# Kernel optimization log

Hardware: AMD Instinct MI355X
Metric: run time of the kernel (lower is better)

Reference implementation:

```python
import jax, jax.numpy as jnp
import numpy as np

B, L, D = 8, 128, 768
DEP, POS = 64, 64
OUT = 768
NEG = -1e30


def setup_inputs() -> dict:
    key = jax.random.key(0)
    ks = jax.random.split(key, 12)
    fan = DEP + POS + D
    s_attn = 1.0 / np.sqrt(fan)
    inp = {
        "text": jax.random.normal(ks[0], (B, L, D), jnp.float32),
        "adj": jax.random.randint(ks[1], (B, L, L), 0, 2, jnp.int32),
        "dep_embed": jax.random.normal(ks[2], (B, L, L, DEP), jnp.float32),
        "pos_embed": jax.random.normal(ks[3], (B, L, POS), jnp.float32),
        # dep_attn Linear(dep+pos+in -> out), split into the three column blocks
        # of the concat order [text | pos | dep]
        "Wt": jax.random.normal(ks[4], (D, OUT), jnp.float32) * s_attn,
        "Wp_attn": jax.random.normal(ks[5], (POS, OUT), jnp.float32) * s_attn,
        "Wd_attn": jax.random.normal(ks[6], (DEP, OUT), jnp.float32) * s_attn,
        "b_attn": jax.random.normal(ks[7], (OUT,), jnp.float32) * s_attn,
        # dep_fc Linear(dep -> out)
        "Wd": jax.random.normal(ks[8], (DEP, OUT), jnp.float32) / np.sqrt(DEP),
        "bd": jax.random.normal(ks[9], (OUT,), jnp.float32) / np.sqrt(DEP),
        # pos_fc Linear(pos -> out)
        "Wp": jax.random.normal(ks[10], (POS, OUT), jnp.float32) / np.sqrt(POS),
        "bp": jax.random.normal(ks[11], (OUT,), jnp.float32) / np.sqrt(POS),
    }
    return inp


def reference(text, adj, dep_embed, pos_embed, Wt, Wp_attn, Wd_attn, b_attn, Wd, bd, Wp, bp):
    # dep_attn(cat([val_us, pos_us, dep_embed])) == sum of per-block linears,
    # with the text/pos parts broadcast along the j (neighbor) axis.
    r = (jnp.einsum('bid,do->bio', text, Wt)[:, :, None, :]
         + jnp.einsum('bip,po->bio', pos_embed, Wp_attn)[:, :, None, :]
         + jnp.einsum('bijd,do->bijo', dep_embed, Wd_attn)
         + b_attn)                                    # [B, L, L, OUT]
    scores = jnp.sum(r, axis=-1) + jnp.where(adj == 0, NEG, 0.0)
    p = jax.nn.softmax(scores, axis=2)                # [B, L, L]
    # output = val_us + pos_fc(pos_us) + dep_fc(dep_embed); weighted-sum over j
    msg = (text[:, :, None, :]
           + (pos_embed @ Wp + bp)[:, :, None, :]
           + jnp.einsum('bijd,do->bijo', dep_embed, Wd) + bd)  # [B, L, L, D]
    output_sum = jnp.einsum('bij,bijo->bio', p, msg)  # [B, L, D]
    return r, output_sum, p
```

## Files before the change

### kernel.cpp

```cpp
#include <hip/hip_runtime.h>
#include <hip/hip_bf16.h>

typedef float v4f __attribute__((ext_vector_type(4)));

__global__ __launch_bounds__(256) void k_wdsum(const float* __restrict__ Wda,
                                               float* __restrict__ wd_sum) {
    int k = blockIdx.x, t = threadIdx.x;
    float s = Wda[k * 768 + t] + Wda[k * 768 + 256 + t] + Wda[k * 768 + 512 + t];
#pragma unroll
    for (int off = 32; off; off >>= 1) s += __shfl_down(s, off, 64);
    __shared__ float red[4];
    if ((t & 63) == 0) red[t >> 6] = s;
    __syncthreads();
    if (t == 0) wd_sum[k] = red[0] + red[1] + red[2] + red[3];
}

__global__ __launch_bounds__(256) void k_tattn(const float* __restrict__ text,
                                               const float* __restrict__ pos,
                                               const float* __restrict__ Wt,
                                               const float* __restrict__ Wpa,
                                               const float* __restrict__ b_attn,
                                               float* __restrict__ t_attn) {
    __shared__ float At[64][68];
    __shared__ float Bt[64][64];
    int t = threadIdx.x;
    int M0 = blockIdx.x * 64, N0 = blockIdx.y * 64;
    int r0 = (t >> 4) * 4, o0 = (t & 15) * 4;
    float acc[16] = {};
    for (int kc = 0; kc < 13; ++kc) {
        __syncthreads();
        for (int f = t * 4; f < 4096; f += 1024) {
            int row = f >> 6, kcol = f & 63;
            float4 v;
            if (kc < 12) v = *(const float4*)&text[(size_t)(M0 + row) * 768 + kc * 64 + kcol];
            else         v = *(const float4*)&pos[(size_t)(M0 + row) * 64 + kcol];
            At[kcol + 0][row] = v.x; At[kcol + 1][row] = v.y;
            At[kcol + 2][row] = v.z; At[kcol + 3][row] = v.w;
        }
        for (int f = t * 4; f < 4096; f += 1024) {
            int kr = f >> 6, oc = f & 63;
            float4 v;
            if (kc < 12) v = *(const float4*)&Wt[(size_t)(kc * 64 + kr) * 768 + N0 + oc];
            else         v = *(const float4*)&Wpa[(size_t)kr * 768 + N0 + oc];
            *(float4*)&Bt[kr][oc] = v;
        }
        __syncthreads();
#pragma unroll 8
        for (int k = 0; k < 64; ++k) {
            float4 a = *(const float4*)&At[k][r0];
            float4 b = *(const float4*)&Bt[k][o0];
            float av[4] = {a.x, a.y, a.z, a.w};
            float bv[4] = {b.x, b.y, b.z, b.w};
#pragma unroll
            for (int i = 0; i < 4; ++i)
#pragma unroll
                for (int j = 0; j < 4; ++j) acc[i * 4 + j] += av[i] * bv[j];
        }
    }
    float4 bias = *(const float4*)&b_attn[N0 + o0];
    float bb[4] = {bias.x, bias.y, bias.z, bias.w};
#pragma unroll
    for (int i = 0; i < 4; ++i) {
        float4 o;
        o.x = acc[i * 4 + 0] + bb[0]; o.y = acc[i * 4 + 1] + bb[1];
        o.z = acc[i * 4 + 2] + bb[2]; o.w = acc[i * 4 + 3] + bb[3];
        *(float4*)&t_attn[(size_t)(M0 + r0 + i) * 768 + N0 + o0] = o;
    }
}

__global__ __launch_bounds__(256) void k_mega(const float* __restrict__ dep,
                                              const int* __restrict__ adj,
                                              const float* __restrict__ Wda,
                                              const float* __restrict__ t_attn,
                                              const float* __restrict__ wd_sum,
                                              float* __restrict__ r_out,
                                              float* __restrict__ out_p,
                                              float* __restrict__ pd_out) {
    __shared__ float dt[64][132];
    __shared__ float wb[64][64];
    __shared__ float wds[64];
    __shared__ float sc[128];
    __shared__ float pv[128];
    __shared__ float pdp[4][64];
    __shared__ float red[8];
    int t = threadIdx.x;
    int bi = blockIdx.x;
    const float* depb = dep + (size_t)bi * (128 * 64);
    for (int f = t * 4; f < 8192; f += 1024) {
        int j = f >> 6, k0 = f & 63;
        float4 v = *(const float4*)&depb[f];
        dt[k0 + 0][j] = v.x; dt[k0 + 1][j] = v.y;
        dt[k0 + 2][j] = v.z; dt[k0 + 3][j] = v.w;
    }
    if (t < 64) wds[t] = wd_sum[t];
    const float* ta = t_attn + (size_t)bi * 768;
    float s = ta[t] + ta[t + 256] + ta[t + 512];
#pragma unroll
    for (int off = 32; off; off >>= 1) s += __shfl_down(s, off, 64);
    if ((t & 63) == 0) red[t >> 6] = s;
    __syncthreads();
    float S_t = red[0] + red[1] + red[2] + red[3];
    if (t < 128) {
        float d = 0.f;
#pragma unroll
        for (int k = 0; k < 64; ++k) d += dt[k][t] * wds[k];
        float v = S_t + d;
        if (adj[(size_t)bi * 128 + t] == 0) v += -1e30f;
        sc[t] = v;
    }
    __syncthreads();
    if (t < 64) {
        float v = fmaxf(sc[t], sc[t + 64]);
#pragma unroll
        for (int off = 32; off; off >>= 1) v = fmaxf(v, __shfl_down(v, off, 64));
        if (t == 0) red[4] = v;
    }
    __syncthreads();
    if (t < 128) pv[t] = __expf(sc[t] - red[4]);
    __syncthreads();
    if (t < 64) {
        float v = pv[t] + pv[t + 64];
#pragma unroll
        for (int off = 32; off; off >>= 1) v += __shfl_down(v, off, 64);
        if (t == 0) red[5] = v;
    }
    __syncthreads();
    float inv = 1.0f / red[5];
    if (t < 128) {
        float pj = pv[t] * inv;
        pv[t] = pj;
        out_p[(size_t)bi * 128 + t] = pj;
    }
    __syncthreads();
    {
        int k = t & 63, seg = t >> 6;
        float a = 0.f;
#pragma unroll
        for (int jj = 0; jj < 32; ++jj) a += pv[seg * 32 + jj] * dt[k][seg * 32 + jj];
        pdp[seg][k] = a;
    }
    __syncthreads();
    if (t < 64) pd_out[(size_t)bi * 64 + t] = pdp[0][t] + pdp[1][t] + pdp[2][t] + pdp[3][t];

    int j0 = (t >> 3) * 4;
    int o0 = (t & 7) * 8;
    float* rb = r_out + (size_t)bi * (128 * 768);
    for (int oc = 0; oc < 12; ++oc) {
        __syncthreads();
        for (int f = t * 4; f < 4096; f += 1024) {
            int k = f >> 6, o = f & 63;
            *(float4*)&wb[k][o] = *(const float4*)&Wda[(size_t)k * 768 + oc * 64 + o];
        }
        __syncthreads();
        float acc[32] = {};
#pragma unroll 4
        for (int k = 0; k < 64; ++k) {
            float4 a  = *(const float4*)&dt[k][j0];
            float4 b0 = *(const float4*)&wb[k][o0];
            float4 b1 = *(const float4*)&wb[k][o0 + 4];
            float av[4] = {a.x, a.y, a.z, a.w};
            float bv[8] = {b0.x, b0.y, b0.z, b0.w, b1.x, b1.y, b1.z, b1.w};
#pragma unroll
            for (int jj = 0; jj < 4; ++jj)
#pragma unroll
                for (int oo = 0; oo < 8; ++oo) acc[jj * 8 + oo] += av[jj] * bv[oo];
        }
        float4 t0 = *(const float4*)&ta[oc * 64 + o0];
        float4 t1 = *(const float4*)&ta[oc * 64 + o0 + 4];
        float tv[8] = {t0.x, t0.y, t0.z, t0.w, t1.x, t1.y, t1.z, t1.w};
#pragma unroll
        for (int jj = 0; jj < 4; ++jj) {
            float* dst = &rb[(size_t)(j0 + jj) * 768 + oc * 64 + o0];
            v4f w0 = {acc[jj * 8 + 0] + tv[0], acc[jj * 8 + 1] + tv[1],
                      acc[jj * 8 + 2] + tv[2], acc[jj * 8 + 3] + tv[3]};
            v4f w1 = {acc[jj * 8 + 4] + tv[4], acc[jj * 8 + 5] + tv[5],
                      acc[jj * 8 + 6] + tv[6], acc[jj * 8 + 7] + tv[7]};
            __builtin_nontemporal_store(w0, (v4f*)dst);
            __builtin_nontemporal_store(w1, (v4f*)(dst + 4));
        }
    }
}

__global__ __launch_bounds__(256) void k_out(const float* __restrict__ text,
                                             const float* __restrict__ pos,
                                             const float* __restrict__ Wp,
                                             const float* __restrict__ bp,
                                             const float* __restrict__ Wd,
                                             const float* __restrict__ bd,
                                             const float* __restrict__ pd,
                                             float* __restrict__ outp) {
    __shared__ float ps[8][64];
    __shared__ float pdl[8][64];
    int t = threadIdx.x;
    int bi0 = blockIdx.x * 8;
    for (int f = t; f < 512; f += 256) {
        int g = f >> 6, k = f & 63;
        ps[g][k]  = pos[(size_t)(bi0 + g) * 64 + k];
        pdl[g][k] = pd[(size_t)(bi0 + g) * 64 + k];
    }
    __syncthreads();
    if (t < 192) {
        int d0 = t * 4;
        float acc[32] = {};
#pragma unroll 4
        for (int k = 0; k < 64; ++k) {
            float4 wp = *(const float4*)&Wp[(size_t)k * 768 + d0];
            float4 wd = *(const float4*)&Wd[(size_t)k * 768 + d0];
            float wpv[4] = {wp.x, wp.y, wp.z, wp.w};
            float wdv[4] = {wd.x, wd.y, wd.z, wd.w};
#pragma unroll
            for (int g = 0; g < 8; ++g) {
                float pk = ps[g][k], dk = pdl[g][k];
#pragma unroll
                for (int c = 0; c < 4; ++c) acc[g * 4 + c] += pk * wpv[c] + dk * wdv[c];
            }
        }
        float4 bpv = *(const float4*)&bp[d0];
        float4 bdv = *(const float4*)&bd[d0];
        float bb[4] = {bpv.x + bdv.x, bpv.y + bdv.y, bpv.z + bdv.z, bpv.w + bdv.w};
#pragma unroll
        for (int g = 0; g < 8; ++g) {
            float4 tx = *(const float4*)&text[(size_t)(bi0 + g) * 768 + d0];
            float4 o;
            o.x = acc[g * 4 + 0] + tx.x + bb[0];
            o.y = acc[g * 4 + 1] + tx.y + bb[1];
            o.z = acc[g * 4 + 2] + tx.z + bb[2];
            o.w = acc[g * 4 + 3] + tx.w + bb[3];
            *(float4*)&outp[(size_t)(bi0 + g) * 768 + d0] = o;
        }
    }
}

extern "C" void kernel_launch(void* const* d_in, const int* in_sizes, int n_in,
                              void* d_out, int out_size, void* d_ws, size_t ws_size,
                              hipStream_t stream) {
    const float* text   = (const float*)d_in[0];
    const int*   adj    = (const int*)d_in[1];
    const float* dep    = (const float*)d_in[2];
    const float* pos    = (const float*)d_in[3];
    const float* Wt     = (const float*)d_in[4];
    const float* Wpa    = (const float*)d_in[5];
    const float* Wda    = (const float*)d_in[6];
    const float* b_attn = (const float*)d_in[7];
    const float* Wd     = (const float*)d_in[8];
    const float* bd     = (const float*)d_in[9];
    const float* Wp     = (const float*)d_in[10];
    const float* bp     = (const float*)d_in[11];

    float* out    = (float*)d_out;
    float* r_out  = out;
    float* os_out = out + (size_t)8 * 128 * 128 * 768;
    float* p_out  = os_out + (size_t)8 * 128 * 768;

    float* ws     = (float*)d_ws;
    float* t_attn = ws;
    float* wd_sum = ws + 786432;
    float* pd     = ws + 786496;

    k_wdsum<<<64, 256, 0, stream>>>(Wda, wd_sum);
    k_tattn<<<dim3(16, 12), 256, 0, stream>>>(text, pos, Wt, Wpa, b_attn, t_attn);
    k_mega<<<1024, 256, 0, stream>>>(dep, adj, Wda, t_attn, wd_sum, r_out, p_out, pd);
    k_out<<<128, 256, 0, stream>>>(text, pos, Wp, bp, Wd, bd, pd, os_out);
}
```

Baseline: 651.2 us.

## Compute dependency-attention projection with bf16 MFMA instead of scalar FP32 FMA

The big dep_embed × Wd_attn product that writes r now runs on bf16 MFMA 16x16x32 instructions. A new pre-pass converts and transposes Wd_attn to bf16, and dep_embed is staged in LDS as bf16. The score and pooled-dep reductions now read fp32 dep straight from global memory, dropping the fp32 transposed LDS tile and the per-chunk weight staging and barriers. Output stores become scalar nontemporal stores in MFMA layout, and using bf16 lowers accuracy, which may exceed the tolerance for r.

After: 621.0 us. 4.6% less time.

```diff
diff --git a/kernel.cpp b/kernel.cpp
--- a/kernel.cpp
+++ b/kernel.cpp
@@ -2,6 +2,13 @@
 #include <hip/hip_bf16.h>
 
 typedef float v4f __attribute__((ext_vector_type(4)));
+typedef short short8 __attribute__((ext_vector_type(8)));
+
+__device__ inline ushort f2bf(float x) {
+    unsigned u = __float_as_uint(x);
+    unsigned r = u + 0x7fffu + ((u >> 16) & 1u);
+    return (ushort)(r >> 16);
+}
 
 __global__ __launch_bounds__(256) void k_wdsum(const float* __restrict__ Wda,
                                                float* __restrict__ wd_sum) {
@@ -13,6 +20,13 @@
     if ((t & 63) == 0) red[t >> 6] = s;
     __syncthreads();
     if (t == 0) wd_sum[k] = red[0] + red[1] + red[2] + red[3];
+}
+
+__global__ __launch_bounds__(256) void k_cvt(const float* __restrict__ Wda,
+                                             ushort* __restrict__ wdat) {
+    int idx = blockIdx.x * 256 + threadIdx.x;
+    int o = idx >> 6, k = idx & 63;
+    wdat[idx] = f2bf(Wda[(size_t)k * 768 + o]);
 }
 
 __global__ __launch_bounds__(256) void k_tattn(const float* __restrict__ text,
@@ -70,14 +84,13 @@
 
 __global__ __launch_bounds__(256) void k_mega(const float* __restrict__ dep,
                                               const int* __restrict__ adj,
-                                              const float* __restrict__ Wda,
+                                              const ushort* __restrict__ wdat,
                                               const float* __restrict__ t_attn,
                                               const float* __restrict__ wd_sum,
                                               float* __restrict__ r_out,
                                               float* __restrict__ out_p,
                                               float* __restrict__ pd_out) {
-    __shared__ float dt[64][132];
-    __shared__ float wb[64][64];
+    __shared__ __align__(16) ushort db[128 * 72];
     __shared__ float wds[64];
     __shared__ float sc[128];
     __shared__ float pv[128];
@@ -86,11 +99,15 @@
     int t = threadIdx.x;
     int bi = blockIdx.x;
     const float* depb = dep + (size_t)bi * (128 * 64);
-    for (int f = t * 4; f < 8192; f += 1024) {
-        int j = f >> 6, k0 = f & 63;
-        float4 v = *(const float4*)&depb[f];
-        dt[k0 + 0][j] = v.x; dt[k0 + 1][j] = v.y;
-        dt[k0 + 2][j] = v.z; dt[k0 + 3][j] = v.w;
+#pragma unroll
+    for (int it = 0; it < 8; ++it) {
+        int f = t + it * 256;
+        int j = f >> 4, k4 = f & 15;
+        float4 v = *(const float4*)&depb[(size_t)f * 4];
+        union { ushort u[4]; uint2 d; } pk;
+        pk.u[0] = f2bf(v.x); pk.u[1] = f2bf(v.y);
+        pk.u[2] = f2bf(v.z); pk.u[3] = f2bf(v.w);
+        *(uint2*)&db[j * 72 + k4 * 4] = pk.d;
     }
     if (t < 64) wds[t] = wd_sum[t];
     const float* ta = t_attn + (size_t)bi * 768;
@@ -101,12 +118,17 @@
     __syncthreads();
     float S_t = red[0] + red[1] + red[2] + red[3];
     if (t < 128) {
+        const float* row = depb + (size_t)t * 64;
         float d = 0.f;
 #pragma unroll
-        for (int k = 0; k < 64; ++k) d += dt[k][t] * wds[k];
-        float v = S_t + d;
-        if (adj[(size_t)bi * 128 + t] == 0) v += -1e30f;
-        sc[t] = v;
+        for (int k4 = 0; k4 < 16; ++k4) {
+            float4 v = *(const float4*)&row[k4 * 4];
+            d += v.x * wds[k4 * 4 + 0] + v.y * wds[k4 * 4 + 1]
+               + v.z * wds[k4 * 4 + 2] + v.w * wds[k4 * 4 + 3];
+        }
+        float sval = S_t + d;
+        if (adj[(size_t)bi * 128 + t] == 0) sval += -1e30f;
+        sc[t] = sval;
     }
     __syncthreads();
     if (t < 64) {
@@ -133,50 +155,48 @@
     }
     __syncthreads();
     {
-        int k = t & 63, seg = t >> 6;
+        int kk = t & 63, seg = t >> 6;
         float a = 0.f;
 #pragma unroll
-        for (int jj = 0; jj < 32; ++jj) a += pv[seg * 32 + jj] * dt[k][seg * 32 + jj];
-        pdp[seg][k] = a;
+        for (int jj = 0; jj < 32; ++jj)
+            a += pv[seg * 32 + jj] * depb[(size_t)(seg * 32 + jj) * 64 + kk];
+        pdp[seg][kk] = a;
     }
     __syncthreads();
     if (t < 64) pd_out[(size_t)bi * 64 + t] = pdp[0][t] + pdp[1][t] + pdp[2][t] + pdp[3][t];
 
-    int j0 = (t >> 3) * 4;
-    int o0 = (t & 7) * 8;
+    int w = t >> 6, l = t & 63;
+    int col = l & 15, q = l >> 4;
+    short8 afr[2][2];
+#pragma unroll
+    for (int jt = 0; jt < 2; ++jt)
+#pragma unroll
+        for (int h = 0; h < 2; ++h)
+            afr[jt][h] = *(const short8*)&db[(w * 32 + jt * 16 + col) * 72 + h * 32 + q * 8];
     float* rb = r_out + (size_t)bi * (128 * 768);
     for (int oc = 0; oc < 12; ++oc) {
-        __syncthreads();
-        for (int f = t * 4; f < 4096; f += 1024) {
-            int k = f >> 6, o = f & 63;
-            *(float4*)&wb[k][o] = *(const float4*)&Wda[(size_t)k * 768 + oc * 64 + o];
-        }
-        __syncthreads();
-        float acc[32] = {};
-#pragma unroll 4
-        for (int k = 0; k < 64; ++k) {
-            float4 a  = *(const float4*)&dt[k][j0];
-            float4 b0 = *(const float4*)&wb[k][o0];
-            float4 b1 = *(const float4*)&wb[k][o0 + 4];
-            float av[4] = {a.x, a.y, a.z, a.w};
-            float bv[8] = {b0.x, b0.y, b0.z, b0.w, b1.x, b1.y, b1.z, b1.w};
-#pragma unroll
-            for (int jj = 0; jj < 4; ++jj)
-#pragma unroll
-                for (int oo = 0; oo < 8; ++oo) acc[jj * 8 + oo] += av[jj] * bv[oo];
-        }
-        float4 t0 = *(const float4*)&ta[oc * 64 + o0];
-        float4 t1 = *(const float4*)&ta[oc * 64 + o0 + 4];
-        float tv[8] = {t0.x, t0.y, t0.z, t0.w, t1.x, t1.y, t1.z, t1.w};
-#pragma unroll
-        for (int jj = 0; jj < 4; ++jj) {
-            float* dst = &rb[(size_t)(j0 + jj) * 768 + oc * 64 + o0];
-            v4f w0 = {acc[jj * 8 + 0] + tv[0], acc[jj * 8 + 1] + tv[1],
-                      acc[jj * 8 + 2] + tv[2], acc[jj * 8 + 3] + tv[3]};
-            v4f w1 = {acc[jj * 8 + 4] + tv[4], acc[jj * 8 + 5] + tv[5],
-                      acc[jj * 8 + 6] + tv[6], acc[jj * 8 + 7] + tv[7]};
-            __builtin_nontemporal_store(w0, (v4f*)dst);
-            __builtin_nontemporal_store(w1, (v4f*)(dst + 4));
+        int O = oc * 64;
+        short8 bfr[4][2];
+#pragma unroll
+        for (int ot = 0; ot < 4; ++ot)
+#pragma unroll
+            for (int h = 0; h < 2; ++h)
+                bfr[ot][h] = *(const short8*)&wdat[(size_t)(O + ot * 16 + col) * 64 + h * 32 + q * 8];
+        float tav[4];
+#pragma unroll
+        for (int ot = 0; ot < 4; ++ot) tav[ot] = ta[O + ot * 16 + col];
+#pragma unroll
+        for (int ot = 0; ot < 4; ++ot) {
+#pragma unroll
+            for (int jt = 0; jt < 2; ++jt) {
+                v4f acc = {0.f, 0.f, 0.f, 0.f};
+                acc = __builtin_amdgcn_mfma_f32_16x16x32_bf16(afr[jt][0], bfr[ot][0], acc, 0, 0, 0);
+                acc = __builtin_amdgcn_mfma_f32_16x16x32_bf16(afr[jt][1], bfr[ot][1], acc, 0, 0, 0);
+                float* dst = rb + (size_t)(w * 32 + jt * 16 + q * 4) * 768 + O + ot * 16 + col;
+#pragma unroll
+                for (int reg = 0; reg < 4; ++reg)
+                    __builtin_nontemporal_store(acc[reg] + tav[ot], dst + (size_t)reg * 768);
+            }
         }
     }
 }
@@ -256,9 +276,11 @@
     float* t_attn = ws;
     float* wd_sum = ws + 786432;
     float* pd     = ws + 786496;
+    ushort* wdat  = (ushort*)(ws + 852032);
 
     k_wdsum<<<64, 256, 0, stream>>>(Wda, wd_sum);
+    k_cvt<<<192, 256, 0, stream>>>(Wda, wdat);
     k_tattn<<<dim3(16, 12), 256, 0, stream>>>(text, pos, Wt, Wpa, b_attn, t_attn);
-    k_mega<<<1024, 256, 0, stream>>>(dep, adj, Wda, t_attn, wd_sum, r_out, p_out, pd);
+    k_mega<<<1024, 256, 0, stream>>>(dep, adj, wdat, t_attn, wd_sum, r_out, p_out, pd);
     k_out<<<128, 256, 0, stream>>>(text, pos, Wp, bp, Wd, bd, pd, os_out);
 }
```
